# Kernel tuning notes

Measured on AMD Instinct MI355X. Metric: run time of the kernel, lower is better.

## Reference

```python
import jax, jax.numpy as jnp
import numpy as np

VOCAB, EMBED_DIM, ENCODE_DIM = 50000, 128, 128
B, N = 512, 500            # trees per batch, nodes per tree
MAX_DEPTH = 40             # static bound on tree depth (uniform-attachment trees stay far below)


def setup_inputs() -> dict:
    rng = np.random.default_rng(0)
    T = B * N
    tokens = rng.integers(0, VOCAB, size=T).astype(np.int64)
    # random recursive trees: node i attaches to a uniformly random earlier node
    u = rng.random((B, N))
    pl = np.floor(u * np.arange(N)).astype(np.int64)  # local parent; node 0 is root
    depth = np.zeros((B, N), dtype=np.int64)
    rows = np.arange(B)
    for i in range(1, N):
        depth[:, i] = depth[rows, pl[:, i]] + 1
    assert depth.max() < MAX_DEPTH
    parent = pl + (np.arange(B)[:, None] * N)
    parent[:, 0] = T  # roots scatter into a dummy row
    node2batch = np.repeat(np.arange(B), N).astype(np.int64)

    key = jax.random.key(0)
    k1, k2, k3 = jax.random.split(key, 3)
    emb = jax.random.normal(k1, (VOCAB, EMBED_DIM), jnp.float32) * 0.02
    Wc = jax.random.normal(k2, (EMBED_DIM, ENCODE_DIM), jnp.float32) * 0.05
    bc = jax.random.normal(k3, (ENCODE_DIM,), jnp.float32) * 0.01
    return {
        "tokens": jnp.asarray(tokens),
        "parent": jnp.asarray(parent.reshape(-1)),
        "depth": jnp.asarray(depth.reshape(-1)),
        "node2batch": jnp.asarray(node2batch),
        "emb": emb, "Wc": Wc, "bc": bc, "bs": B,
    }


def reference(tokens, parent, depth, node2batch, emb, Wc, bc, bs):
    T = tokens.shape[0]
    # per-node W_c(embedding(token))  [T, D]
    x = emb[tokens] @ Wc + bc
    # bottom-up subtree sums: v(n) = sum_{m in subtree(n)} x[m]
    v = jnp.concatenate([x, jnp.zeros((1, x.shape[1]), x.dtype)], axis=0)  # +1 dummy row
    for d in range(MAX_DEPTH, 0, -1):
        contrib = jnp.where((depth == d)[:, None], v[:T], jnp.zeros((), x.dtype))
        v = v.at[parent].add(contrib)  # depth-d nodes push into depth d-1 parents
    node_vals = v[:T]
    # per-tree elementwise max over node values (node_list max-pool)
    out = jax.ops.segment_max(node_vals, node2batch, num_segments=bs)
    # rows absent from a node_list entry are zero, so the pool includes 0
    return jnp.maximum(out, jnp.zeros((), out.dtype))
```

## Files before the change

### kernel.cpp

```cpp
#include <hip/hip_runtime.h>
#include <hip/hip_bf16.h>

#define B_BATCH 512
#define NPB     500
#define DIM     128
#define VOCAB   50000
#define MAXD    40
#define NPREP   512
#define NGEMM   ((VOCAB + 63) / 64)

typedef short bf16x8 __attribute__((ext_vector_type(8)));
typedef float f32x4  __attribute__((ext_vector_type(4)));

__device__ __forceinline__ unsigned short f2bf(float x) {
    unsigned u = __float_as_uint(x);
    return (unsigned short)((u + 0x7fffu + ((u >> 16) & 1u)) >> 16);
}

__global__ __launch_bounds__(256) void prep_gemm(const int* __restrict__ tokens,
                                                 const int* __restrict__ parent,
                                                 const int* __restrict__ depth,
                                                 const float* __restrict__ emb,
                                                 const float* __restrict__ Wc,
                                                 const float* __restrict__ bc,
                                                 int* __restrict__ tokD,
                                                 unsigned short* __restrict__ endD,
                                                 unsigned short* __restrict__ Eb) {
    const int tid = threadIdx.x;

    if (blockIdx.x >= NPREP) {
        __shared__ __align__(16) unsigned short WcT[DIM * 32];

        const int lane = tid & 63, w = tid >> 6;
        const int q = lane >> 4, mc = lane & 15;
        const int rowBase = (blockIdx.x - NPREP) * 64;
        const int arow = min(rowBase + w * 16 + mc, VOCAB - 1);

        f32x4 acc[8];
        #pragma unroll
        for (int nt = 0; nt < 8; ++nt) acc[nt] = (f32x4){0.f, 0.f, 0.f, 0.f};

        const int kk = tid >> 3;
        const int c0 = (tid & 7) * 16;

        #pragma unroll
        for (int kc = 0; kc < 4; ++kc) {
            const float* wsrc = &Wc[(kc * 32 + kk) * DIM + c0];
            float wv[16];
            *(float4*)(wv + 0)  = *(const float4*)(wsrc + 0);
            *(float4*)(wv + 4)  = *(const float4*)(wsrc + 4);
            *(float4*)(wv + 8)  = *(const float4*)(wsrc + 8);
            *(float4*)(wv + 12) = *(const float4*)(wsrc + 12);
            __syncthreads();
            #pragma unroll
            for (int i = 0; i < 16; ++i)
                WcT[(c0 + i) * 32 + kk] = f2bf(wv[i]);
            __syncthreads();

            const float* src = &emb[(long long)arow * DIM + kc * 32 + q * 8];
            float4 v0 = *(const float4*)src;
            float4 v1 = *(const float4*)(src + 4);
            unsigned short aw[8] = {f2bf(v0.x), f2bf(v0.y), f2bf(v0.z), f2bf(v0.w),
                                    f2bf(v1.x), f2bf(v1.y), f2bf(v1.z), f2bf(v1.w)};
            bf16x8 a = *(bf16x8*)aw;

            #pragma unroll
            for (int nt = 0; nt < 8; ++nt) {
                bf16x8 bfr = *(bf16x8*)&WcT[(nt * 16 + mc) * 32 + q * 8];
                acc[nt] = __builtin_amdgcn_mfma_f32_16x16x32_bf16(a, bfr, acc[nt], 0, 0, 0);
            }
        }

        #pragma unroll
        for (int nt = 0; nt < 8; ++nt) {
            float bcv = bc[nt * 16 + mc];
            #pragma unroll
            for (int r = 0; r < 4; ++r) {
                int grow = rowBase + w * 16 + q * 4 + r;
                if (grow < VOCAB)
                    Eb[(long long)grow * DIM + nt * 16 + mc] = f2bf(acc[nt][r] + bcv);
            }
        }
        return;
    }

    __shared__ unsigned short parL[NPB];
    __shared__ unsigned short depL[NPB];
    __shared__ int   tokL[NPB];
    __shared__ int   sizeL[NPB];
    __shared__ int   childCur[NPB];
    __shared__ unsigned short sibp[NPB];
    __shared__ unsigned short tinL[NPB];
    __shared__ unsigned short bucket[NPB];
    __shared__ int hist[MAXD + 1], off[MAXD + 1], cur[MAXD + 1];
    __shared__ int tmpTok[NPB];
    __shared__ unsigned short tmpEnd[NPB];
    __shared__ int sdmax;

    const int b = blockIdx.x;
    const long long base = (long long)b * NPB;

    if (tid <= MAXD) hist[tid] = 0;
    __syncthreads();
    for (int n = tid; n < NPB; n += 256) {
        int d = depth[base + n];
        depL[n]  = (unsigned short)d;
        parL[n]  = (unsigned short)(n == 0 ? 0 : (int)(parent[base + n] - base));
        tokL[n]  = tokens[base + n];
        sizeL[n] = 1;
        childCur[n] = 0;
        if (n > 0) atomicAdd(&hist[d], 1);
    }
    __syncthreads();

    if (tid < 64) {
        int h = (tid >= 1 && tid <= MAXD) ? hist[tid] : 0;
        int x = h;
        #pragma unroll
        for (int o = 1; o < 64; o <<= 1) { int y = __shfl_up(x, o, 64); if (tid >= o) x += y; }
        if (tid >= 1 && tid <= MAXD) { off[tid] = x - h; cur[tid] = x - h; }
        int dm = (h > 0) ? tid : 0;
        #pragma unroll
        for (int o = 32; o; o >>= 1) dm = max(dm, __shfl_down(dm, o));
        if (tid == 0) sdmax = dm;
    }
    __syncthreads();

    for (int n = 1 + tid; n < NPB; n += 256)
        bucket[atomicAdd(&cur[depL[n]], 1)] = (unsigned short)n;
    __syncthreads();
    const int dmax = sdmax;

    for (int d = dmax; d >= 1; --d) {
        int c = hist[d], o = off[d];
        for (int i = tid; i < c; i += 256) {
            int n = bucket[o + i];
            atomicAdd(&sizeL[parL[n]], sizeL[n]);
        }
        __syncthreads();
    }

    for (int n = 1 + tid; n < NPB; n += 256)
        sibp[n] = (unsigned short)atomicAdd(&childCur[parL[n]], sizeL[n]);
    if (tid == 0) tinL[0] = 0;
    __syncthreads();

    for (int d = 1; d <= dmax; ++d) {
        int c = hist[d], o = off[d];
        for (int i = tid; i < c; i += 256) {
            int n = bucket[o + i];
            tinL[n] = (unsigned short)((int)tinL[parL[n]] + 1 + (int)sibp[n]);
        }
        __syncthreads();
    }

    for (int n = tid; n < NPB; n += 256) {
        int t = tinL[n];
        tmpTok[t] = tokL[n];
        tmpEnd[t] = (unsigned short)(t + sizeL[n] - 1);
    }
    __syncthreads();
    for (int t = tid; t < NPB; t += 256) {
        tokD[base + t] = tmpTok[t];
        endD[base + t] = tmpEnd[t];
    }
}

__global__ __launch_bounds__(1024) void scan_k(const int* __restrict__ tokD,
                                               const unsigned short* __restrict__ endD,
                                               const unsigned short* __restrict__ Eb,
                                               float* __restrict__ out) {
    const int b = blockIdx.x & 511, sp = blockIdx.x >> 9, tid = threadIdx.x;
    const long long base = (long long)b * NPB;
    __shared__ unsigned short Sbf[NPB * 64];
    __shared__ unsigned short endL[NPB];
    __shared__ float partials[16 * 64];
    __shared__ float wmax[16 * 64];

    #pragma unroll
    for (int u = 0; u < 4; ++u) {
        int n = (tid >> 3) + u * 128;
        if (n < NPB) {
            int tok = tokD[base + n];
            const unsigned short* g = &Eb[(long long)tok * DIM + sp * 64 + (tid & 7) * 8];
            __builtin_amdgcn_global_load_lds(
                (const __attribute__((address_space(1))) void*)g,
                (__attribute__((address_space(3))) void*)&Sbf[n * 64 + (tid & 7) * 8],
                16, 0, 0);
        }
    }
    if (tid < NPB) endL[tid] = endD[base + tid];
    __syncthreads();

    const int j = tid & 63, c = tid >> 6;
    float x[32];
    {
        float run = 0.f;
        #pragma unroll
        for (int k = 0; k < 32; ++k) {
            int t = c * 32 + k;
            float v = (t < NPB)
                ? __uint_as_float((unsigned)Sbf[t * 64 + j] << 16) : 0.f;
            run += v; x[k] = run;
        }
        partials[c * 64 + j] = run;
    }
    __syncthreads();
    float off = 0.f;
    for (int cc = 0; cc < c; ++cc) off += partials[cc * 64 + j];
    #pragma unroll
    for (int k = 0; k < 32; ++k) {
        int t = c * 32 + k;
        x[k] += off;
        if (t < NPB) Sbf[t * 64 + j] = f2bf(x[k]);
    }
    __syncthreads();

    float m = -INFINITY;
    #pragma unroll
    for (int k = 0; k < 32; ++k) {
        int t = c * 32 + k;
        if (t < NPB) {
            float hi = __uint_as_float((unsigned)Sbf[(int)endL[t] * 64 + j] << 16);
            float lo = (k > 0) ? x[k - 1] : off;
            m = fmaxf(m, hi - lo);
        }
    }
    wmax[c * 64 + j] = m;
    __syncthreads();
    if (tid < 64) {
        float mm = wmax[tid];
        #pragma unroll
        for (int w = 1; w < 16; ++w) mm = fmaxf(mm, wmax[w * 64 + tid]);
        out[b * DIM + sp * 64 + tid] = fmaxf(mm, 0.0f);
    }
}

extern "C" void kernel_launch(void* const* d_in, const int* in_sizes, int n_in,
                              void* d_out, int out_size, void* d_ws, size_t ws_size,
                              hipStream_t stream) {
    const int*   tokens = (const int*)d_in[0];
    const int*   parent = (const int*)d_in[1];
    const int*   depth  = (const int*)d_in[2];
    const float* emb    = (const float*)d_in[4];
    const float* Wc     = (const float*)d_in[5];
    const float* bc     = (const float*)d_in[6];
    float*       out    = (float*)d_out;

    unsigned short* Eb   = (unsigned short*)d_ws;
    int*            tokD = (int*)(Eb + (long long)VOCAB * DIM);
    unsigned short* endD = (unsigned short*)(tokD + B_BATCH * NPB);

    prep_gemm<<<NPREP + NGEMM, 256, 0, stream>>>(tokens, parent, depth,
                                                 emb, Wc, bc, tokD, endD, Eb);
    scan_k<<<B_BATCH * 2, 1024, 0, stream>>>(tokD, endD, Eb, out);
}
```

Measured before the change: 124.6 us.

## Preload GEMM operands and stage all Wc slices with one barrier; union shared memory

The GEMM branch of prep_gemm now issues all embedding-row loads up front and writes all four transposed Wc k-slices into shared memory before a single barrier, then runs all MFMAs. This replaces the per-k-chunk double barrier and should overlap global loads with conversion. Shared memory is unioned through one 32KB buffer so the tree-prep branch and the GEMM branch no longer add their allocations together. scan_k also gets a minimum-blocks hint in launch_bounds, which may limit registers.

```diff
diff --git a/kernel.cpp b/kernel.cpp
--- a/kernel.cpp
+++ b/kernel.cpp
@@ -16,6 +16,21 @@
     unsigned u = __float_as_uint(x);
     return (unsigned short)((u + 0x7fffu + ((u >> 16) & 1u)) >> 16);
 }
+
+struct PrepShm {
+    int   tokL[NPB];
+    int   sizeL[NPB];
+    int   childCur[NPB];
+    int   tmpTok[NPB];
+    int   hist[MAXD + 1], off[MAXD + 1], cur[MAXD + 1];
+    int   sdmax;
+    unsigned short parL[NPB];
+    unsigned short depL[NPB];
+    unsigned short sibp[NPB];
+    unsigned short tinL[NPB];
+    unsigned short bucket[NPB];
+    unsigned short tmpEnd[NPB];
+};
 
 __global__ __launch_bounds__(256) void prep_gemm(const int* __restrict__ tokens,
                                                  const int* __restrict__ parent,
@@ -26,48 +41,61 @@
                                                  int* __restrict__ tokD,
                                                  unsigned short* __restrict__ endD,
                                                  unsigned short* __restrict__ Eb) {
+    __shared__ __align__(16) unsigned char shm[32768];
     const int tid = threadIdx.x;
 
     if (blockIdx.x >= NPREP) {
-        __shared__ __align__(16) unsigned short WcT[DIM * 32];
+        unsigned short* WcT4 = (unsigned short*)shm;
 
         const int lane = tid & 63, w = tid >> 6;
         const int q = lane >> 4, mc = lane & 15;
         const int rowBase = (blockIdx.x - NPREP) * 64;
         const int arow = min(rowBase + w * 16 + mc, VOCAB - 1);
 
-        f32x4 acc[8];
-        #pragma unroll
-        for (int nt = 0; nt < 8; ++nt) acc[nt] = (f32x4){0.f, 0.f, 0.f, 0.f};
+        const float* esrc = &emb[(long long)arow * DIM];
+        float4 ev[8];
+        #pragma unroll
+        for (int kc = 0; kc < 4; ++kc) {
+            const float* src = esrc + kc * 32 + q * 8;
+            ev[2 * kc]     = *(const float4*)src;
+            ev[2 * kc + 1] = *(const float4*)(src + 4);
+        }
 
         const int kk = tid >> 3;
         const int c0 = (tid & 7) * 16;
-
-        #pragma unroll
-        for (int kc = 0; kc < 4; ++kc) {
-            const float* wsrc = &Wc[(kc * 32 + kk) * DIM + c0];
+        #pragma unroll
+        for (int s = 0; s < 4; ++s) {
+            const float* wsrc = &Wc[(s * 32 + kk) * DIM + c0];
             float wv[16];
             *(float4*)(wv + 0)  = *(const float4*)(wsrc + 0);
             *(float4*)(wv + 4)  = *(const float4*)(wsrc + 4);
             *(float4*)(wv + 8)  = *(const float4*)(wsrc + 8);
             *(float4*)(wv + 12) = *(const float4*)(wsrc + 12);
-            __syncthreads();
             #pragma unroll
             for (int i = 0; i < 16; ++i)
-                WcT[(c0 + i) * 32 + kk] = f2bf(wv[i]);
-            __syncthreads();
-
-            const float* src = &emb[(long long)arow * DIM + kc * 32 + q * 8];
-            float4 v0 = *(const float4*)src;
-            float4 v1 = *(const float4*)(src + 4);
+                WcT4[s * 4096 + (c0 + i) * 32 + kk] = f2bf(wv[i]);
+        }
+
+        bf16x8 a4[4];
+        #pragma unroll
+        for (int kc = 0; kc < 4; ++kc) {
+            float4 v0 = ev[2 * kc], v1 = ev[2 * kc + 1];
             unsigned short aw[8] = {f2bf(v0.x), f2bf(v0.y), f2bf(v0.z), f2bf(v0.w),
                                     f2bf(v1.x), f2bf(v1.y), f2bf(v1.z), f2bf(v1.w)};
-            bf16x8 a = *(bf16x8*)aw;
-
+            a4[kc] = *(bf16x8*)aw;
+        }
+        __syncthreads();
+
+        f32x4 acc[8];
+        #pragma unroll
+        for (int nt = 0; nt < 8; ++nt) acc[nt] = (f32x4){0.f, 0.f, 0.f, 0.f};
+
+        #pragma unroll
+        for (int kc = 0; kc < 4; ++kc) {
             #pragma unroll
             for (int nt = 0; nt < 8; ++nt) {
-                bf16x8 bfr = *(bf16x8*)&WcT[(nt * 16 + mc) * 32 + q * 8];
-                acc[nt] = __builtin_amdgcn_mfma_f32_16x16x32_bf16(a, bfr, acc[nt], 0, 0, 0);
+                bf16x8 bfr = *(bf16x8*)&WcT4[kc * 4096 + (nt * 16 + mc) * 32 + q * 8];
+                acc[nt] = __builtin_amdgcn_mfma_f32_16x16x32_bf16(a4[kc], bfr, acc[nt], 0, 0, 0);
             }
         }
 
@@ -84,92 +112,81 @@
         return;
     }
 
-    __shared__ unsigned short parL[NPB];
-    __shared__ unsigned short depL[NPB];
-    __shared__ int   tokL[NPB];
-    __shared__ int   sizeL[NPB];
-    __shared__ int   childCur[NPB];
-    __shared__ unsigned short sibp[NPB];
-    __shared__ unsigned short tinL[NPB];
-    __shared__ unsigned short bucket[NPB];
-    __shared__ int hist[MAXD + 1], off[MAXD + 1], cur[MAXD + 1];
-    __shared__ int tmpTok[NPB];
-    __shared__ unsigned short tmpEnd[NPB];
-    __shared__ int sdmax;
+    PrepShm& P = *(PrepShm*)shm;
 
     const int b = blockIdx.x;
     const long long base = (long long)b * NPB;
 
-    if (tid <= MAXD) hist[tid] = 0;
+    if (tid <= MAXD) P.hist[tid] = 0;
     __syncthreads();
     for (int n = tid; n < NPB; n += 256) {
         int d = depth[base + n];
-        depL[n]  = (unsigned short)d;
-        parL[n]  = (unsigned short)(n == 0 ? 0 : (int)(parent[base + n] - base));
-        tokL[n]  = tokens[base + n];
-        sizeL[n] = 1;
-        childCur[n] = 0;
-        if (n > 0) atomicAdd(&hist[d], 1);
+        P.depL[n]  = (unsigned short)d;
+        P.parL[n]  = (unsigned short)(n == 0 ? 0 : (int)(parent[base + n] - base));
+        P.tokL[n]  = tokens[base + n];
+        P.sizeL[n] = 1;
+        P.childCur[n] = 0;
+        if (n > 0) atomicAdd(&P.hist[d], 1);
     }
     __syncthreads();
 
     if (tid < 64) {
-        int h = (tid >= 1 && tid <= MAXD) ? hist[tid] : 0;
+        int h = (tid >= 1 && tid <= MAXD) ? P.hist[tid] : 0;
         int x = h;
         #pragma unroll
         for (int o = 1; o < 64; o <<= 1) { int y = __shfl_up(x, o, 64); if (tid >= o) x += y; }
-        if (tid >= 1 && tid <= MAXD) { off[tid] = x - h; cur[tid] = x - h; }
+        if (tid >= 1 && tid <= MAXD) { P.off[tid] = x - h; P.cur[tid] = x - h; }
         int dm = (h > 0) ? tid : 0;
         #pragma unroll
         for (int o = 32; o; o >>= 1) dm = max(dm, __shfl_down(dm, o));
-        if (tid == 0) sdmax = dm;
+        if (tid == 0) P.sdmax = dm;
     }
     __syncthreads();
 
     for (int n = 1 + tid; n < NPB; n += 256)
-        bucket[atomicAdd(&cur[depL[n]], 1)] = (unsigned short)n;
-    __syncthreads();
-    const int dmax = sdmax;
+        P.bucket[atomicAdd(&P.cur[P.depL[n]], 1)] = (unsigned short)n;
+    __syncthreads();
+    const int dmax = P.sdmax;
 
     for (int d = dmax; d >= 1; --d) {
-        int c = hist[d], o = off[d];
+        int c = P.hist[d], o = P.off[d];
         for (int i = tid; i < c; i += 256) {
-            int n = bucket[o + i];
-            atomicAdd(&sizeL[parL[n]], sizeL[n]);
+            int n = P.bucket[o + i];
+            atomicAdd(&P.sizeL[P.parL[n]], P.sizeL[n]);
         }
         __syncthreads();
     }
 
     for (int n = 1 + tid; n < NPB; n += 256)
-        sibp[n] = (unsigned short)atomicAdd(&childCur[parL[n]], sizeL[n]);
-    if (tid == 0) tinL[0] = 0;
+        P.sibp[n] = (unsigned short)atomicAdd(&P.childCur[P.parL[n]], P.sizeL[n]);
+    if (tid == 0) P.tinL[0] = 0;
     __syncthreads();
 
     for (int d = 1; d <= dmax; ++d) {
-        int c = hist[d], o = off[d];
+        int c = P.hist[d], o = P.off[d];
         for (int i = tid; i < c; i += 256) {
-            int n = bucket[o + i];
-            tinL[n] = (unsigned short)((int)tinL[parL[n]] + 1 + (int)sibp[n]);
+            int n = P.bucket[o + i];
+            P.tinL[n] = (unsigned short)((int)P.tinL[P.parL[n]] + 1 + (int)P.sibp[n]);
         }
         __syncthreads();
     }
 
     for (int n = tid; n < NPB; n += 256) {
-        int t = tinL[n];
-        tmpTok[t] = tokL[n];
-        tmpEnd[t] = (unsigned short)(t + sizeL[n] - 1);
+        int t = P.tinL[n];
+        P.tmpTok[t] = P.tokL[n];
+        P.tmpEnd[t] = (unsigned short)(t + P.sizeL[n] - 1);
     }
     __syncthreads();
     for (int t = tid; t < NPB; t += 256) {
-        tokD[base + t] = tmpTok[t];
-        endD[base + t] = tmpEnd[t];
-    }
-}
-
-__global__ __launch_bounds__(1024) void scan_k(const int* __restrict__ tokD,
-                                               const unsigned short* __restrict__ endD,
-                                               const unsigned short* __restrict__ Eb,
-                                               float* __restrict__ out) {
+        tokD[base + t] = P.tmpTok[t];
+        endD[base + t] = P.tmpEnd[t];
+    }
+}
+
+__global__ __launch_bounds__(1024, 8) void scan_k(const int* __restrict__ tokD,
+                                                  const unsigned short* __restrict__ endD,
+                                                  const unsigned short* __restrict__ Eb,
+                                                  float* __restrict__ out) {
     const int b = blockIdx.x & 511, sp = blockIdx.x >> 9, tid = threadIdx.x;
     const long long base = (long long)b * NPB;
     __shared__ unsigned short Sbf[NPB * 64];
```

Measured after the change: 137.1 us. 1.1x slower.

## Replace level-synchronous tree traversal with per-node ancestor walks in prep

Applied to the files above, without the earlier changes.

The per-tree preprocessing no longer builds a depth histogram and buckets and no longer steps level by level with a barrier per depth. Each thread now walks its node's ancestor chain: it atomically increments every ancestor's subtree size, then sums sibling offsets along the path to get the preorder index. Shared memory is also unioned between the GEMM branch and the prep branch to shrink the per-block LDS footprint. This removes up to two barriers per depth level, in exchange for O(depth) serial work per thread and more atomic contention near the root.

```diff
diff --git a/kernel.cpp b/kernel.cpp
--- a/kernel.cpp
+++ b/kernel.cpp
@@ -16,6 +16,16 @@
     unsigned u = __float_as_uint(x);
     return (unsigned short)((u + 0x7fffu + ((u >> 16) & 1u)) >> 16);
 }
+
+struct PrepShm {
+    int   tokL[NPB];
+    int   sizeL[NPB];
+    int   childCur[NPB];
+    int   tmpTok[NPB];
+    unsigned short parL[NPB];
+    unsigned short sibp[NPB];
+    unsigned short tmpEnd[NPB];
+};
 
 __global__ __launch_bounds__(256) void prep_gemm(const int* __restrict__ tokens,
                                                  const int* __restrict__ parent,
@@ -26,10 +36,11 @@
                                                  int* __restrict__ tokD,
                                                  unsigned short* __restrict__ endD,
                                                  unsigned short* __restrict__ Eb) {
+    __shared__ __align__(16) unsigned char shm[11264];
     const int tid = threadIdx.x;
 
     if (blockIdx.x >= NPREP) {
-        __shared__ __align__(16) unsigned short WcT[DIM * 32];
+        unsigned short* WcT = (unsigned short*)shm;
 
         const int lane = tid & 63, w = tid >> 6;
         const int q = lane >> 4, mc = lane & 15;
@@ -84,85 +95,60 @@
         return;
     }
 
-    __shared__ unsigned short parL[NPB];
-    __shared__ unsigned short depL[NPB];
-    __shared__ int   tokL[NPB];
-    __shared__ int   sizeL[NPB];
-    __shared__ int   childCur[NPB];
-    __shared__ unsigned short sibp[NPB];
-    __shared__ unsigned short tinL[NPB];
-    __shared__ unsigned short bucket[NPB];
-    __shared__ int hist[MAXD + 1], off[MAXD + 1], cur[MAXD + 1];
-    __shared__ int tmpTok[NPB];
-    __shared__ unsigned short tmpEnd[NPB];
-    __shared__ int sdmax;
+    PrepShm& P = *(PrepShm*)shm;
 
     const int b = blockIdx.x;
     const long long base = (long long)b * NPB;
 
-    if (tid <= MAXD) hist[tid] = 0;
-    __syncthreads();
-    for (int n = tid; n < NPB; n += 256) {
-        int d = depth[base + n];
-        depL[n]  = (unsigned short)d;
-        parL[n]  = (unsigned short)(n == 0 ? 0 : (int)(parent[base + n] - base));
-        tokL[n]  = tokens[base + n];
-        sizeL[n] = 1;
-        childCur[n] = 0;
-        if (n > 0) atomicAdd(&hist[d], 1);
-    }
-    __syncthreads();
-
-    if (tid < 64) {
-        int h = (tid >= 1 && tid <= MAXD) ? hist[tid] : 0;
-        int x = h;
-        #pragma unroll
-        for (int o = 1; o < 64; o <<= 1) { int y = __shfl_up(x, o, 64); if (tid >= o) x += y; }
-        if (tid >= 1 && tid <= MAXD) { off[tid] = x - h; cur[tid] = x - h; }
-        int dm = (h > 0) ? tid : 0;
-        #pragma unroll
-        for (int o = 32; o; o >>= 1) dm = max(dm, __shfl_down(dm, o));
-        if (tid == 0) sdmax = dm;
-    }
-    __syncthreads();
-
-    for (int n = 1 + tid; n < NPB; n += 256)
-        bucket[atomicAdd(&cur[depL[n]], 1)] = (unsigned short)n;
-    __syncthreads();
-    const int dmax = sdmax;
-
-    for (int d = dmax; d >= 1; --d) {
-        int c = hist[d], o = off[d];
-        for (int i = tid; i < c; i += 256) {
-            int n = bucket[o + i];
-            atomicAdd(&sizeL[parL[n]], sizeL[n]);
-        }
-        __syncthreads();
-    }
-
-    for (int n = 1 + tid; n < NPB; n += 256)
-        sibp[n] = (unsigned short)atomicAdd(&childCur[parL[n]], sizeL[n]);
-    if (tid == 0) tinL[0] = 0;
-    __syncthreads();
-
-    for (int d = 1; d <= dmax; ++d) {
-        int c = hist[d], o = off[d];
-        for (int i = tid; i < c; i += 256) {
-            int n = bucket[o + i];
-            tinL[n] = (unsigned short)((int)tinL[parL[n]] + 1 + (int)sibp[n]);
-        }
-        __syncthreads();
-    }
-
-    for (int n = tid; n < NPB; n += 256) {
-        int t = tinL[n];
-        tmpTok[t] = tokL[n];
-        tmpEnd[t] = (unsigned short)(t + sizeL[n] - 1);
-    }
-    __syncthreads();
+    const int n0 = tid, n1 = tid + 256;
+    int d0 = 0, d1 = 0;
+    {
+        d0 = (int)depth[base + n0];
+        P.parL[n0]     = (unsigned short)(n0 == 0 ? 0 : (int)(parent[base + n0] - base));
+        P.tokL[n0]     = tokens[base + n0];
+        P.sizeL[n0]    = 1;
+        P.childCur[n0] = 0;
+        if (n1 < NPB) {
+            d1 = (int)depth[base + n1];
+            P.parL[n1]     = (unsigned short)(int)(parent[base + n1] - base);
+            P.tokL[n1]     = tokens[base + n1];
+            P.sizeL[n1]    = 1;
+            P.childCur[n1] = 0;
+        }
+    }
+    __syncthreads();
+
+    if (n0 >= 1) {
+        int p = P.parL[n0];
+        while (p != 0) { atomicAdd(&P.sizeL[p], 1); p = P.parL[p]; }
+    }
+    if (n1 < NPB) {
+        int p = P.parL[n1];
+        while (p != 0) { atomicAdd(&P.sizeL[p], 1); p = P.parL[p]; }
+    }
+    __syncthreads();
+
+    if (n0 >= 1) P.sibp[n0] = (unsigned short)atomicAdd(&P.childCur[P.parL[n0]], P.sizeL[n0]);
+    if (n1 < NPB) P.sibp[n1] = (unsigned short)atomicAdd(&P.childCur[P.parL[n1]], P.sizeL[n1]);
+    __syncthreads();
+
+    {
+        int t = d0, a = n0;
+        while (a != 0) { t += P.sibp[a]; a = P.parL[a]; }
+        P.tmpTok[t] = P.tokL[n0];
+        P.tmpEnd[t] = (unsigned short)(n0 == 0 ? NPB - 1 : t + P.sizeL[n0] - 1);
+    }
+    if (n1 < NPB) {
+        int t = d1, a = n1;
+        while (a != 0) { t += P.sibp[a]; a = P.parL[a]; }
+        P.tmpTok[t] = P.tokL[n1];
+        P.tmpEnd[t] = (unsigned short)(t + P.sizeL[n1] - 1);
+    }
+    __syncthreads();
+
     for (int t = tid; t < NPB; t += 256) {
-        tokD[base + t] = tmpTok[t];
-        endD[base + t] = tmpEnd[t];
+        tokD[base + t] = P.tmpTok[t];
+        endD[base + t] = P.tmpEnd[t];
     }
 }
 
```

Result: no change. 126.0 us (+1.2%).
